# Performance work log

Hardware: AMD Instinct MI355X
Metric: run time of the kernel (lower is better)

Reference implementation:

```python
import jax, jax.numpy as jnp
import numpy as np

B, C, N = 8, 512, 2048
C8 = C // 8


def setup_inputs() -> dict:
    key = jax.random.key(0)
    kx, kq, kk, kv, kg = jax.random.split(key, 5)
    return {
        "x": jax.random.normal(kx, (B, C, N), dtype=jnp.float32),
        "Wq": jax.random.normal(kq, (C8, C), dtype=jnp.float32) * (1.0 / np.sqrt(C)),
        "Wk": jax.random.normal(kk, (C8, C), dtype=jnp.float32) * (1.0 / np.sqrt(C)),
        "Wv": jax.random.normal(kv, (C, C), dtype=jnp.float32) * (1.0 / np.sqrt(C)),
        # torch init is gamma=0.0; use a small random value so the attention
        # branch contributes to the output.
        "gamma": jax.random.uniform(kg, (1,), dtype=jnp.float32),
    }


def reference(x, Wq, Wk, Wv, gamma):
    # 1x1 convs == per-position linear maps over channels
    f = jnp.einsum("oc,bcn->bon", Wq, x)   # [B, C/8, N]
    g = jnp.einsum("oc,bcn->bon", Wk, x)   # [B, C/8, N]
    h = jnp.einsum("oc,bcn->bon", Wv, x)   # [B, C,   N]
    # scores[b,n,m] = sum_c f[b,c,n] * g[b,c,m]  (unscaled, as in source)
    scores = jnp.einsum("bcn,bcm->bnm", f, g)  # [B, N, N]
    # softmax over dim=1 (the query-position axis) — atypical but faithful
    beta = jax.nn.softmax(scores, axis=1)
    # o = gamma * h @ beta + x
    o = gamma[0] * jnp.einsum("bcn,bnm->bcm", h, beta) + x
    return o
```

## Files before the change

### kernel.cpp

```cpp
#include <hip/hip_runtime.h>
#include <hip/hip_bf16.h>
#include <math.h>

#define NB 8
#define NC 512
#define NN 2048

typedef unsigned short u16;
typedef __attribute__((ext_vector_type(8))) short short8;
typedef __attribute__((ext_vector_type(4))) float f32x4;

__device__ __forceinline__ float bf16_to_f32(u16 v) {
  union { unsigned int u; float f; } c; c.u = ((unsigned int)v) << 16; return c.f;
}
__device__ __forceinline__ u16 f32_to_bf16(float f) {
  __hip_bfloat16 h = __float2bfloat16(f);
  union { __hip_bfloat16 h; u16 u; } c; c.h = h; return c.u;
}
__device__ __forceinline__ void split2(float v, unsigned short& hi, unsigned short& lo) {
  hi = f32_to_bf16(v);
  lo = f32_to_bf16(v - bf16_to_f32(hi));
}

__device__ __forceinline__ void gl_lds16(const void* g, void* l) {
  __builtin_amdgcn_global_load_lds(
      (const __attribute__((address_space(1))) unsigned int*)g,
      (__attribute__((address_space(3))) unsigned int*)l, 16, 0, 0);
}

__device__ __forceinline__ void stage128x32(const u16* __restrict__ src, size_t row_base,
                                            int selems, int k0, u16* lds, int tid) {
#pragma unroll
  for (int s = 0; s < 2; ++s) {
    int flat = s * 4096 + tid * 16;
    int row = flat >> 6;
    int kb  = flat & 63;
    const char* g = (const char*)(src + (row_base + row) * (size_t)selems + k0) + kb;
    u16* l = lds + s * 2048 + (tid & ~63) * 8;
    gl_lds16(g, l);
  }
}

__global__ __launch_bounds__(256)
void wsplit_kernel(const float* __restrict__ Wq, const float* __restrict__ Wk,
                   const float* __restrict__ Wv, u16* __restrict__ Whi,
                   u16* __restrict__ Wlo) {
  int idx = (blockIdx.x * 256 + threadIdx.x) * 4;
  int r = idx >> 9, c = idx & 511;
  const float* src;
  if (r < 64)       src = Wq + (size_t)r * NC + c;
  else if (r < 128) src = Wk + (size_t)(r - 64) * NC + c;
  else              src = Wv + (size_t)(r - 128) * NC + c;
  float4 v = *(const float4*)src;
  ushort4 hi, lo;
  split2(v.x, hi.x, lo.x); split2(v.y, hi.y, lo.y);
  split2(v.z, hi.z, lo.z); split2(v.w, hi.w, lo.w);
  *(ushort4*)&Whi[idx] = hi;
  *(ushort4*)&Wlo[idx] = lo;
}

__global__ __launch_bounds__(256)
void xsplit_kernel(const float* __restrict__ x, u16* __restrict__ xThi,
                   u16* __restrict__ xTlo) {
  const int b = blockIdx.z, c0 = blockIdx.y * 64, n0 = blockIdx.x * 64;
  __shared__ float t[64][65];
  const int tid = threadIdx.x, tx = tid & 15, ty = tid >> 4;
#pragma unroll
  for (int r = 0; r < 4; ++r) {
    int c = r * 16 + ty;
    float4 v = *(const float4*)&x[((size_t)b * NC + c0 + c) * NN + n0 + tx * 4];
    t[c][tx * 4 + 0] = v.x; t[c][tx * 4 + 1] = v.y;
    t[c][tx * 4 + 2] = v.z; t[c][tx * 4 + 3] = v.w;
  }
  __syncthreads();
#pragma unroll
  for (int r = 0; r < 4; ++r) {
    int n = r * 16 + ty;
    ushort4 hi, lo;
    split2(t[tx * 4 + 0][n], hi.x, lo.x);
    split2(t[tx * 4 + 1][n], hi.y, lo.y);
    split2(t[tx * 4 + 2][n], hi.z, lo.z);
    split2(t[tx * 4 + 3][n], hi.w, lo.w);
    size_t off = ((size_t)b * NN + n0 + n) * NC + c0 + tx * 4;
    *(ushort4*)&xThi[off] = hi;
    *(ushort4*)&xTlo[off] = lo;
  }
}

__global__ __launch_bounds__(256)
void proj_mfma_kernel(const u16* __restrict__ xThi, const u16* __restrict__ xTlo,
                      const u16* __restrict__ Whi, const u16* __restrict__ Wlo,
                      u16* __restrict__ fgThi, u16* __restrict__ fgTlo,
                      u16* __restrict__ hw) {
  const int b  = blockIdx.z;
  const int n0 = blockIdx.x * 128;
  const int r0 = blockIdx.y * 128;
  const bool fg = (r0 == 0);

  __shared__ u16 Wh[2][128 * 32], Wl[2][128 * 32], Xh[2][128 * 32], Xl[2][128 * 32];

  const int tid = threadIdx.x, wave = tid >> 6, lane = tid & 63;
  const int quad = lane >> 4, l16 = lane & 15;
  const int wa = (wave >> 1) * 64, wb = (wave & 1) * 64;
  const size_t xrow = (size_t)b * NN + n0;

  f32x4 acc[4][4];
#pragma unroll
  for (int i = 0; i < 4; ++i)
#pragma unroll
    for (int j = 0; j < 4; ++j) acc[i][j] = (f32x4){0.f, 0.f, 0.f, 0.f};

  stage128x32(Whi, r0, NC, 0, Wh[0], tid);
  stage128x32(xThi, xrow, NC, 0, Xh[0], tid);
  if (fg) {
    stage128x32(Wlo, r0, NC, 0, Wl[0], tid);
    stage128x32(xTlo, xrow, NC, 0, Xl[0], tid);
  }

  const int KIT = NC / 32;
  for (int ki = 0; ki < KIT; ++ki) {
    __syncthreads();
    if (ki + 1 < KIT) {
      const int nb = (ki + 1) & 1, k1 = (ki + 1) * 32;
      stage128x32(Whi, r0, NC, k1, Wh[nb], tid);
      stage128x32(xThi, xrow, NC, k1, Xh[nb], tid);
      if (fg) {
        stage128x32(Wlo, r0, NC, k1, Wl[nb], tid);
        stage128x32(xTlo, xrow, NC, k1, Xl[nb], tid);
      }
    }
    const int cur = ki & 1;

    if (fg) {
      short8 ah[4], al[4], bh[4], bl[4];
#pragma unroll
      for (int i = 0; i < 4; ++i) {
        ah[i] = *(short8*)&Wh[cur][(wa + i * 16 + l16) * 32 + quad * 8];
        al[i] = *(short8*)&Wl[cur][(wa + i * 16 + l16) * 32 + quad * 8];
      }
#pragma unroll
      for (int j = 0; j < 4; ++j) {
        bh[j] = *(short8*)&Xh[cur][(wb + j * 16 + l16) * 32 + quad * 8];
        bl[j] = *(short8*)&Xl[cur][(wb + j * 16 + l16) * 32 + quad * 8];
      }
#pragma unroll
      for (int i = 0; i < 4; ++i)
#pragma unroll
        for (int j = 0; j < 4; ++j) {
          acc[i][j] = __builtin_amdgcn_mfma_f32_16x16x32_bf16(ah[i], bh[j], acc[i][j], 0, 0, 0);
          acc[i][j] = __builtin_amdgcn_mfma_f32_16x16x32_bf16(ah[i], bl[j], acc[i][j], 0, 0, 0);
          acc[i][j] = __builtin_amdgcn_mfma_f32_16x16x32_bf16(al[i], bh[j], acc[i][j], 0, 0, 0);
        }
    } else {
      short8 ah[4], bh[4];
#pragma unroll
      for (int i = 0; i < 4; ++i)
        ah[i] = *(short8*)&Xh[cur][(wa + i * 16 + l16) * 32 + quad * 8];
#pragma unroll
      for (int j = 0; j < 4; ++j)
        bh[j] = *(short8*)&Wh[cur][(wb + j * 16 + l16) * 32 + quad * 8];
#pragma unroll
      for (int i = 0; i < 4; ++i)
#pragma unroll
        for (int j = 0; j < 4; ++j)
          acc[i][j] = __builtin_amdgcn_mfma_f32_16x16x32_bf16(ah[i], bh[j], acc[i][j], 0, 0, 0);
    }
  }

  if (fg) {
#pragma unroll
    for (int i = 0; i < 4; ++i)
#pragma unroll
      for (int j = 0; j < 4; ++j) {
        int rb = wa + i * 16 + quad * 4;
        int n  = n0 + wb + j * 16 + l16;
        ushort4 hi, lo;
        split2(acc[i][j][0], hi.x, lo.x); split2(acc[i][j][1], hi.y, lo.y);
        split2(acc[i][j][2], hi.z, lo.z); split2(acc[i][j][3], hi.w, lo.w);
        size_t off = ((size_t)b * NN + n) * 128 + rb;
        *(ushort4*)&fgThi[off] = hi;
        *(ushort4*)&fgTlo[off] = lo;
      }
  } else {
#pragma unroll
    for (int i = 0; i < 4; ++i)
#pragma unroll
      for (int j = 0; j < 4; ++j) {
        int nb = n0 + wa + i * 16 + quad * 4;
        int c  = r0 - 128 + wb + j * 16 + l16;
        ushort4 hi;
        hi.x = f32_to_bf16(acc[i][j][0]); hi.y = f32_to_bf16(acc[i][j][1]);
        hi.z = f32_to_bf16(acc[i][j][2]); hi.w = f32_to_bf16(acc[i][j][3]);
        *(ushort4*)&hw[((size_t)b * NC + c) * NN + nb] = hi;
      }
  }
}

__global__ __launch_bounds__(512)
void attn_out_kernel(const u16* __restrict__ fgThi, const u16* __restrict__ fgTlo,
                     const u16* __restrict__ hw, const float* __restrict__ x,
                     const float* __restrict__ gamma, float* __restrict__ out) {
  const int s = blockIdx.x;
  const int xcd = s & 7;
  const int t = s >> 3;
  const int mt = t & 15;
  const int hi5 = t >> 4;
  const int p = (hi5 << 3) | xcd;
  const int b = p >> 1;
  const int ch = p & 1;
  const int m0 = mt * 128;
  const int c0 = ch * 256;

  __shared__ u16 Fh[2][64 * 64], Fl[2][64 * 64];
  __shared__ u16 Hs[2][256 * 64];
  __shared__ u16 Ps[2][128 * 64];
  __shared__ float Dn[128];

  const int tid = threadIdx.x, wave = tid >> 6, lane = tid & 63;
  const int quad = lane >> 4, l16 = lane & 15;
  const int ws_n = (wave >> 2) * 32, ws_m = (wave & 3) * 32;
  const int wv_c = (wave >> 1) * 64, wv_m = (wave & 1) * 64;

  const size_t frow = (size_t)b * NN;
  const size_t hrow = (size_t)b * NC + c0;

  short8 gh[2][2], gl[2][2];
#pragma unroll
  for (int j = 0; j < 2; ++j)
#pragma unroll
    for (int k = 0; k < 2; ++k) {
      size_t o = (frow + m0 + ws_m + j * 16 + l16) * 128 + 64 + k * 32 + quad * 8;
      gh[j][k] = *(const short8*)&fgThi[o];
      gl[j][k] = *(const short8*)&fgTlo[o];
    }

  {
    int flat = tid * 16;
    int row = flat >> 7, chunk = (flat >> 4) & 7;
    int kb = ((chunk ^ (row & 7)) << 4);
    gl_lds16((const char*)(fgThi + (frow + row) * 128) + kb, Fh[0] + (tid & ~63) * 8);
    gl_lds16((const char*)(fgTlo + (frow + row) * 128) + kb, Fl[0] + (tid & ~63) * 8);
  }

  float dsum0 = 0.f, dsum1 = 0.f;
  f32x4 ao[4][4];
#pragma unroll
  for (int i = 0; i < 4; ++i)
#pragma unroll
    for (int j = 0; j < 4; ++j) ao[i][j] = (f32x4){0.f, 0.f, 0.f, 0.f};

  const int NT = NN / 64;
  for (int it = 0; it < NT; ++it) {
    const int cur = it & 1;
    __syncthreads();

    if (it + 1 < NT) {
      const int n1 = (it + 1) * 64;
      int flat = tid * 16;
      int row = flat >> 7, chunk = (flat >> 4) & 7;
      int kb = ((chunk ^ (row & 7)) << 4);
      gl_lds16((const char*)(fgThi + (frow + n1 + row) * 128) + kb,
               Fh[cur ^ 1] + (tid & ~63) * 8);
      gl_lds16((const char*)(fgTlo + (frow + n1 + row) * 128) + kb,
               Fl[cur ^ 1] + (tid & ~63) * 8);
    }
    {
      const int n1 = it * 64;
#pragma unroll
      for (int s2 = 0; s2 < 4; ++s2) {
        int f2 = s2 * 8192 + tid * 16;
        int r2 = f2 >> 7, c2 = (f2 >> 4) & 7;
        gl_lds16((const char*)(hw + (hrow + r2) * NN + n1) + ((c2 ^ (r2 & 7)) << 4),
                 Hs[cur] + s2 * 4096 + (tid & ~63) * 8);
      }
    }

    if (it > 0) {
      const int prv = cur ^ 1;
#pragma unroll
      for (int k = 0; k < 2; ++k) {
        short8 hh[4], pb[4];
#pragma unroll
        for (int i = 0; i < 4; ++i) {
          int rr = wv_c + i * 16 + l16;
          hh[i] = *(short8*)&Hs[prv][rr * 64 + ((((k * 4 + quad)) ^ (rr & 7)) << 3)];
        }
#pragma unroll
        for (int j = 0; j < 4; ++j) {
          int rm = wv_m + j * 16 + l16;
          pb[j] = *(short8*)&Ps[prv][rm * 64 + ((((k * 4 + quad)) ^ (rm & 7)) << 3)];
        }
#pragma unroll
        for (int i = 0; i < 4; ++i)
#pragma unroll
          for (int j = 0; j < 4; ++j)
            ao[i][j] = __builtin_amdgcn_mfma_f32_16x16x32_bf16(hh[i], pb[j], ao[i][j], 0, 0, 0);
      }
    }

    f32x4 as[2][2];
#pragma unroll
    for (int i = 0; i < 2; ++i)
#pragma unroll
      for (int j = 0; j < 2; ++j) as[i][j] = (f32x4){0.f, 0.f, 0.f, 0.f};
#pragma unroll
    for (int k = 0; k < 2; ++k) {
      short8 fh[2], fl[2];
#pragma unroll
      for (int i = 0; i < 2; ++i) {
        int rr = ws_n + i * 16 + l16;
        int ci = (((k * 4 + quad) ^ (rr & 7)) << 3);
        fh[i] = *(short8*)&Fh[cur][rr * 64 + ci];
        fl[i] = *(short8*)&Fl[cur][rr * 64 + ci];
      }
#pragma unroll
      for (int i = 0; i < 2; ++i)
#pragma unroll
        for (int j = 0; j < 2; ++j) {
          as[i][j] = __builtin_amdgcn_mfma_f32_16x16x32_bf16(fh[i], gh[j][k], as[i][j], 0, 0, 0);
          as[i][j] = __builtin_amdgcn_mfma_f32_16x16x32_bf16(fh[i], gl[j][k], as[i][j], 0, 0, 0);
          as[i][j] = __builtin_amdgcn_mfma_f32_16x16x32_bf16(fl[i], gh[j][k], as[i][j], 0, 0, 0);
        }
    }

#pragma unroll
    for (int j = 0; j < 2; ++j) {
      int m = ws_m + j * 16 + l16;
#pragma unroll
      for (int i = 0; i < 2; ++i) {
        float e0 = __expf(as[i][j][0]);
        float e1 = __expf(as[i][j][1]);
        float e2 = __expf(as[i][j][2]);
        float e3 = __expf(as[i][j][3]);
        if (j == 0) dsum0 += (e0 + e1) + (e2 + e3);
        else        dsum1 += (e0 + e1) + (e2 + e3);
        ushort4 pk;
        pk.x = f32_to_bf16(e0); pk.y = f32_to_bf16(e1);
        pk.z = f32_to_bf16(e2); pk.w = f32_to_bf16(e3);
        int nb = ws_n * 2 + i * 32 + quad * 8;
        int chunk = nb >> 4;
        int off = (nb & 15) >> 1;
        *(ushort4*)&Ps[cur][m * 64 + ((chunk ^ (m & 7)) << 3) + off] = pk;
      }
    }
  }

  __syncthreads();
  {
    const int prv = (NT - 1) & 1;
#pragma unroll
    for (int k = 0; k < 2; ++k) {
      short8 hh[4], pb[4];
#pragma unroll
      for (int i = 0; i < 4; ++i) {
        int rr = wv_c + i * 16 + l16;
        hh[i] = *(short8*)&Hs[prv][rr * 64 + ((((k * 4 + quad)) ^ (rr & 7)) << 3)];
      }
#pragma unroll
      for (int j = 0; j < 4; ++j) {
        int rm = wv_m + j * 16 + l16;
        pb[j] = *(short8*)&Ps[prv][rm * 64 + ((((k * 4 + quad)) ^ (rm & 7)) << 3)];
      }
#pragma unroll
      for (int i = 0; i < 4; ++i)
#pragma unroll
        for (int j = 0; j < 4; ++j)
          ao[i][j] = __builtin_amdgcn_mfma_f32_16x16x32_bf16(hh[i], pb[j], ao[i][j], 0, 0, 0);
    }
  }

  dsum0 += __shfl_xor(dsum0, 16); dsum0 += __shfl_xor(dsum0, 32);
  dsum1 += __shfl_xor(dsum1, 16); dsum1 += __shfl_xor(dsum1, 32);
  if (tid < 128) Dn[tid] = 0.f;
  __syncthreads();
  if (quad == 0) {
    atomicAdd(&Dn[ws_m + l16], dsum0);
    atomicAdd(&Dn[ws_m + 16 + l16], dsum1);
  }
  __syncthreads();

  const float g = gamma[0];
  float invd[4];
#pragma unroll
  for (int j = 0; j < 4; ++j)
    invd[j] = g / Dn[wv_m + j * 16 + l16];

#pragma unroll
  for (int i = 0; i < 4; ++i) {
#pragma unroll
    for (int j = 0; j < 4; ++j) {
      const int c = c0 + wv_c + i * 16 + quad * 4;
      const int m = m0 + wv_m + j * 16 + l16;
#pragma unroll
      for (int r = 0; r < 4; ++r) {
        size_t off = ((size_t)b * NC + c + r) * NN + m;
        out[off] = fmaf(invd[j], ao[i][j][r], x[off]);
      }
    }
  }
}

extern "C" void kernel_launch(void* const* d_in, const int* in_sizes, int n_in,
                              void* d_out, int out_size, void* d_ws, size_t ws_size,
                              hipStream_t stream) {
  const float* x     = (const float*)d_in[0];
  const float* Wq    = (const float*)d_in[1];
  const float* Wk    = (const float*)d_in[2];
  const float* Wv    = (const float*)d_in[3];
  const float* gamma = (const float*)d_in[4];
  float* out = (float*)d_out;

  char* ws = (char*)d_ws;
  u16*   xThi  = (u16*)ws;
  u16*   xTlo  = (u16*)(ws + 16777216);
  u16*   Whi   = (u16*)(ws + 33554432);
  u16*   Wlo   = (u16*)(ws + 34209792);
  u16*   fgThi = (u16*)(ws + 67108864);
  u16*   fgTlo = (u16*)(ws + 71303168);
  u16*   hw    = (u16*)(ws + 75497472);

  wsplit_kernel<<<dim3(320), 256, 0, stream>>>(Wq, Wk, Wv, Whi, Wlo);
  xsplit_kernel<<<dim3(NN / 64, NC / 64, NB), 256, 0, stream>>>(x, xThi, xTlo);
  proj_mfma_kernel<<<dim3(NN / 128, 5, NB), 256, 0, stream>>>(
      xThi, xTlo, Whi, Wlo, fgThi, fgTlo, hw);
  attn_out_kernel<<<dim3(256), 512, 0, stream>>>(fgThi, fgTlo, hw, x, gamma, out);
}
```

Baseline: 205.1 us.

## Split attention output over four channel chunks and drop the P-tile software pipeline

```diff
diff --git a/kernel.cpp b/kernel.cpp
--- a/kernel.cpp
+++ b/kernel.cpp
@@ -204,22 +204,22 @@
   const int xcd = s & 7;
   const int t = s >> 3;
   const int mt = t & 15;
-  const int hi5 = t >> 4;
-  const int p = (hi5 << 3) | xcd;
-  const int b = p >> 1;
-  const int ch = p & 1;
+  const int ci4 = t >> 4;
+  const int combo = (ci4 << 3) | xcd;
+  const int b = combo >> 2;
+  const int ch = combo & 3;
   const int m0 = mt * 128;
-  const int c0 = ch * 256;
+  const int c0 = ch * 128;
 
   __shared__ u16 Fh[2][64 * 64], Fl[2][64 * 64];
-  __shared__ u16 Hs[2][256 * 64];
-  __shared__ u16 Ps[2][128 * 64];
-  __shared__ float Dn[128];
+  __shared__ u16 Hs[2][128 * 64];
+  __shared__ u16 Ps[128 * 64];
+  float* Dn = (float*)Ps;
 
   const int tid = threadIdx.x, wave = tid >> 6, lane = tid & 63;
   const int quad = lane >> 4, l16 = lane & 15;
   const int ws_n = (wave >> 2) * 32, ws_m = (wave & 3) * 32;
-  const int wv_c = (wave >> 1) * 64, wv_m = (wave & 1) * 64;
+  const int wv_c = (wave >> 2) * 64, wv_m = (wave & 3) * 32;
 
   const size_t frow = (size_t)b * NN;
   const size_t hrow = (size_t)b * NC + c0;
@@ -240,20 +240,26 @@
     int kb = ((chunk ^ (row & 7)) << 4);
     gl_lds16((const char*)(fgThi + (frow + row) * 128) + kb, Fh[0] + (tid & ~63) * 8);
     gl_lds16((const char*)(fgTlo + (frow + row) * 128) + kb, Fl[0] + (tid & ~63) * 8);
-  }
+#pragma unroll
+    for (int s2 = 0; s2 < 2; ++s2) {
+      int f2 = s2 * 8192 + tid * 16;
+      int r2 = f2 >> 7, c2 = (f2 >> 4) & 7;
+      gl_lds16((const char*)(hw + (hrow + r2) * NN) + ((c2 ^ (r2 & 7)) << 4),
+               Hs[0] + s2 * 4096 + (tid & ~63) * 8);
+    }
+  }
+  __syncthreads();
 
   float dsum0 = 0.f, dsum1 = 0.f;
-  f32x4 ao[4][4];
+  f32x4 ao[4][2];
 #pragma unroll
   for (int i = 0; i < 4; ++i)
 #pragma unroll
-    for (int j = 0; j < 4; ++j) ao[i][j] = (f32x4){0.f, 0.f, 0.f, 0.f};
+    for (int j = 0; j < 2; ++j) ao[i][j] = (f32x4){0.f, 0.f, 0.f, 0.f};
 
   const int NT = NN / 64;
   for (int it = 0; it < NT; ++it) {
     const int cur = it & 1;
-    __syncthreads();
-
     if (it + 1 < NT) {
       const int n1 = (it + 1) * 64;
       int flat = tid * 16;
@@ -263,38 +269,12 @@
                Fh[cur ^ 1] + (tid & ~63) * 8);
       gl_lds16((const char*)(fgTlo + (frow + n1 + row) * 128) + kb,
                Fl[cur ^ 1] + (tid & ~63) * 8);
-    }
-    {
-      const int n1 = it * 64;
-#pragma unroll
-      for (int s2 = 0; s2 < 4; ++s2) {
+#pragma unroll
+      for (int s2 = 0; s2 < 2; ++s2) {
         int f2 = s2 * 8192 + tid * 16;
         int r2 = f2 >> 7, c2 = (f2 >> 4) & 7;
         gl_lds16((const char*)(hw + (hrow + r2) * NN + n1) + ((c2 ^ (r2 & 7)) << 4),
-                 Hs[cur] + s2 * 4096 + (tid & ~63) * 8);
-      }
-    }
-
-    if (it > 0) {
-      const int prv = cur ^ 1;
-#pragma unroll
-      for (int k = 0; k < 2; ++k) {
-        short8 hh[4], pb[4];
-#pragma unroll
-        for (int i = 0; i < 4; ++i) {
-          int rr = wv_c + i * 16 + l16;
-          hh[i] = *(short8*)&Hs[prv][rr * 64 + ((((k * 4 + quad)) ^ (rr & 7)) << 3)];
-        }
-#pragma unroll
-        for (int j = 0; j < 4; ++j) {
-          int rm = wv_m + j * 16 + l16;
-          pb[j] = *(short8*)&Ps[prv][rm * 64 + ((((k * 4 + quad)) ^ (rm & 7)) << 3)];
-        }
-#pragma unroll
-        for (int i = 0; i < 4; ++i)
-#pragma unroll
-          for (int j = 0; j < 4; ++j)
-            ao[i][j] = __builtin_amdgcn_mfma_f32_16x16x32_bf16(hh[i], pb[j], ao[i][j], 0, 0, 0);
+                 Hs[cur ^ 1] + s2 * 4096 + (tid & ~63) * 8);
       }
     }
 
@@ -340,33 +320,34 @@
         int nb = ws_n * 2 + i * 32 + quad * 8;
         int chunk = nb >> 4;
         int off = (nb & 15) >> 1;
-        *(ushort4*)&Ps[cur][m * 64 + ((chunk ^ (m & 7)) << 3) + off] = pk;
-      }
-    }
-  }
-
-  __syncthreads();
-  {
-    const int prv = (NT - 1) & 1;
+        *(ushort4*)&Ps[m * 64 + ((chunk ^ (m & 7)) << 3) + off] = pk;
+      }
+    }
+
+    asm volatile("s_waitcnt lgkmcnt(0)" ::: "memory");
+    __builtin_amdgcn_s_barrier();
+
 #pragma unroll
     for (int k = 0; k < 2; ++k) {
-      short8 hh[4], pb[4];
+      short8 hh[4], pb[2];
 #pragma unroll
       for (int i = 0; i < 4; ++i) {
         int rr = wv_c + i * 16 + l16;
-        hh[i] = *(short8*)&Hs[prv][rr * 64 + ((((k * 4 + quad)) ^ (rr & 7)) << 3)];
-      }
-#pragma unroll
-      for (int j = 0; j < 4; ++j) {
+        hh[i] = *(short8*)&Hs[cur][rr * 64 + ((((k * 4 + quad)) ^ (rr & 7)) << 3)];
+      }
+#pragma unroll
+      for (int j = 0; j < 2; ++j) {
         int rm = wv_m + j * 16 + l16;
-        pb[j] = *(short8*)&Ps[prv][rm * 64 + ((((k * 4 + quad)) ^ (rm & 7)) << 3)];
+        pb[j] = *(short8*)&Ps[rm * 64 + ((((k * 4 + quad)) ^ (rm & 7)) << 3)];
       }
 #pragma unroll
       for (int i = 0; i < 4; ++i)
 #pragma unroll
-        for (int j = 0; j < 4; ++j)
+        for (int j = 0; j < 2; ++j)
           ao[i][j] = __builtin_amdgcn_mfma_f32_16x16x32_bf16(hh[i], pb[j], ao[i][j], 0, 0, 0);
     }
+
+    __syncthreads();
   }
 
   dsum0 += __shfl_xor(dsum0, 16); dsum0 += __shfl_xor(dsum0, 32);
@@ -380,15 +361,15 @@
   __syncthreads();
 
   const float g = gamma[0];
-  float invd[4];
-#pragma unroll
-  for (int j = 0; j < 4; ++j)
+  float invd[2];
+#pragma unroll
+  for (int j = 0; j < 2; ++j)
     invd[j] = g / Dn[wv_m + j * 16 + l16];
 
 #pragma unroll
   for (int i = 0; i < 4; ++i) {
 #pragma unroll
-    for (int j = 0; j < 4; ++j) {
+    for (int j = 0; j < 2; ++j) {
       const int c = c0 + wv_c + i * 16 + quad * 4;
       const int m = m0 + wv_m + j * 16 + l16;
 #pragma unroll
@@ -423,5 +404,5 @@
   xsplit_kernel<<<dim3(NN / 64, NC / 64, NB), 256, 0, stream>>>(x, xThi, xTlo);
   proj_mfma_kernel<<<dim3(NN / 128, 5, NB), 256, 0, stream>>>(
       xThi, xTlo, Whi, Wlo, fgThi, fgTlo, hw);
-  attn_out_kernel<<<dim3(256), 512, 0, stream>>>(fgThi, fgTlo, hw, x, gamma, out);
-}
+  attn_out_kernel<<<dim3(512), 512, 0, stream>>>(fgThi, fgTlo, hw, x, gamma, out);
+}
```

New measurement: 211.2 us. 3.0% more time.
